# Performance work log

Hardware: AMD Instinct MI355X
Metric: run time of the kernel (lower is better)

Reference implementation:

```python
import math
import jax, jax.numpy as jnp
import numpy as np

B, N, D, H = 2, 2048, 1024, 16
HD = D // H  # 64
TWO_PI = 2.0 * math.pi
ROPE_BASE = 10000.0


def setup_inputs() -> dict:
    key = jax.random.key(0)
    ks = jax.random.split(key, 8)
    s = 0.02
    x = jax.random.normal(ks[0], (B, N, D), dtype=jnp.float32)
    Wq = jax.random.normal(ks[1], (D, D), dtype=jnp.float32) * s
    Wk = jax.random.normal(ks[2], (D, D), dtype=jnp.float32) * s
    Wv = jax.random.normal(ks[3], (D, D), dtype=jnp.float32) * s
    Wo = jax.random.normal(ks[4], (D, D), dtype=jnp.float32) * s
    cw = jax.random.normal(ks[5], (D,), dtype=jnp.float32) * s  # complexity_proj weight
    cb = jnp.zeros((), dtype=jnp.float32)                        # complexity_proj bias
    alpha = jnp.asarray(0.1, dtype=jnp.float32)
    T_base = jnp.asarray(10.0, dtype=jnp.float32)
    root_ids = jax.random.randint(ks[6], (B, N), 0, 1000)
    mask = jnp.tril(jnp.ones((N, N), dtype=jnp.int32))  # causal
    return {"x": x, "Wq": Wq, "Wk": Wk, "Wv": Wv, "Wo": Wo,
            "alpha": alpha, "T_base": T_base, "cw": cw, "cb": cb,
            "root_ids": root_ids, "mask": mask, "t_step": 3}


def _rope_cos_sin(seq_len, head_dim, dtype):
    inv_freq = 1.0 / (ROPE_BASE ** (jnp.arange(0, head_dim, 2, dtype=jnp.float32) / head_dim))
    pos = jnp.arange(seq_len, dtype=jnp.float32)
    freqs = pos[:, None] * inv_freq[None, :]          # (N, HD/2)
    emb = jnp.concatenate([freqs, freqs], axis=-1)    # (N, HD)
    return jnp.cos(emb).astype(dtype), jnp.sin(emb).astype(dtype)


def _rotate_half(t):
    half = t.shape[-1] // 2
    return jnp.concatenate([-t[..., half:], t[..., :half]], axis=-1)


def reference(x, Wq, Wk, Wv, Wo, alpha, T_base, cw, cb, root_ids, mask, t_step):
    b, n, d = x.shape
    # QKV projection -> (B, H, N, HD)
    def proj(W):
        return jnp.einsum('bnd,ed->bne', x, W).reshape(b, n, H, HD).transpose(0, 2, 1, 3)
    q, k, v = proj(Wq), proj(Wk), proj(Wv)
    # RoPE
    cos, sin = _rope_cos_sin(n, HD, x.dtype)          # (N, HD)
    q = q * cos + _rotate_half(q) * sin
    k = k * cos + _rotate_half(k) * sin
    # Per-sample temperature via complexity + cardiac oscillation
    complexity = jax.nn.sigmoid(jnp.einsum('bd,d->b', x.mean(axis=1), cw) + cb)  # (B,)
    T_eff = (jnp.abs(T_base) + 1.0) * (0.5 + complexity)                          # (B,)
    psi = 1.0 + alpha * jnp.sin(TWO_PI * t_step / T_eff)                          # (B,)
    scale = (math.sqrt(HD) * psi)[:, None, None, None]                            # (B,1,1,1)
    # Attention with full NxN scores (eager path, as in source)
    scores = jnp.einsum('bhqd,bhkd->bhqk', q, k) / scale
    scores = jnp.where(mask[None, None, :, :] == 0, -jnp.inf, scores)
    attn = jax.nn.softmax(scores, axis=-1)
    out = jnp.einsum('bhqk,bhkd->bhqd', attn, v)       # (B,H,N,HD)
    out = out.transpose(0, 2, 1, 3).reshape(b, n, d)
    return jnp.einsum('bnd,ed->bne', out, Wo)
```

## Files before the change

### kernel.cpp

```cpp
#include <hip/hip_runtime.h>


typedef short short8 __attribute__((ext_vector_type(8)));
typedef float floatx4 __attribute__((ext_vector_type(4)));
typedef float f32x16 __attribute__((ext_vector_type(16)));
typedef unsigned int uint4v __attribute__((ext_vector_type(4)));
typedef unsigned int u32x4v __attribute__((ext_vector_type(4)));
typedef unsigned short us4 __attribute__((ext_vector_type(4)));
typedef unsigned short u16;

#define DEV __device__ __forceinline__

static const int Bb = 2;

static const size_t OFF_XB = 0;
static const size_t OFF_WQ = 8388608;
static const size_t OFF_WK = OFF_WQ + 2097152;
static const size_t OFF_WV = OFF_WK + 2097152;
static const size_t OFF_WO = OFF_WV + 2097152;
static const size_t OFF_Q  = OFF_WO + 2097152;
static const size_t OFF_K  = OFF_Q + 8388608;
static const size_t OFF_V  = OFF_K + 8388608;
static const size_t OFF_AO = OFF_V + 8388608;
static const size_t OFF_SC = OFF_AO + 8388608;

DEV u16 f2bf(float f) {
  unsigned int u = __builtin_bit_cast(unsigned int, f);
  u += 0x7fffu + ((u >> 16) & 1u);
  return (u16)(u >> 16);
}

DEV unsigned pkbf(float lo, float hi) {
  unsigned r;
  asm("v_cvt_pk_bf16_f32 %0, %1, %2" : "=v"(r) : "v"(lo), "v"(hi));
  return r;
}

__global__ __launch_bounds__(256) void cvt_all_kernel(
    const float* __restrict__ x, const float* __restrict__ wq,
    const float* __restrict__ wk, const float* __restrict__ wv,
    const float* __restrict__ wo, const float* __restrict__ cw,
    u16* __restrict__ xb, u16* __restrict__ wqb, u16* __restrict__ wkb,
    u16* __restrict__ wvb, u16* __restrict__ wob, float* __restrict__ part) {
  const int blk = blockIdx.x;
  if (blk < 4096) {
    int i = blk * 256 + threadIdx.x;
    float4 f = ((const float4*)x)[i];
    us4 o;
    o[0] = f2bf(f.x); o[1] = f2bf(f.y); o[2] = f2bf(f.z); o[3] = f2bf(f.w);
    ((us4*)xb)[i] = o;
    float4 c = ((const float4*)cw)[i & 255];
    float acc = f.x * c.x + f.y * c.y + f.z * c.z + f.w * c.w;
    __shared__ float red[256];
    red[threadIdx.x] = acc;
    __syncthreads();
    for (int s = 128; s > 0; s >>= 1) {
      if (threadIdx.x < s) red[threadIdx.x] += red[threadIdx.x + s];
      __syncthreads();
    }
    if (threadIdx.x == 0) part[blk] = red[0];
  } else {
    int r = blk - 4096;
    int wi = r >> 10;
    int i = (r & 1023) * 256 + threadIdx.x;
    const float* src = (wi == 0) ? wq : (wi == 1) ? wk : (wi == 2) ? wv : wo;
    u16* dst = (wi == 0) ? wqb : (wi == 1) ? wkb : (wi == 2) ? wvb : wob;
    float4 f = ((const float4*)src)[i];
    us4 o;
    o[0] = f2bf(f.x); o[1] = f2bf(f.y); o[2] = f2bf(f.z); o[3] = f2bf(f.w);
    ((us4*)dst)[i] = o;
  }
}

__global__ void scale_finalize_kernel(const float* __restrict__ part,
                                      const float* __restrict__ cb,
                                      const float* __restrict__ alpha,
                                      const float* __restrict__ tb,
                                      const int* __restrict__ tstep,
                                      float* __restrict__ out) {
  const int b = threadIdx.x >> 7, t = threadIdx.x & 127;
  float s = 0.f;
  for (int i = t; i < 2048; i += 128) s += part[b * 2048 + i];
  __shared__ float red[2][128];
  red[b][t] = s;
  __syncthreads();
  for (int st = 64; st > 0; st >>= 1) {
    if (t < st) red[b][t] += red[b][t + st];
    __syncthreads();
  }
  if (t == 0) {
    float sm = red[b][0] * (1.0f / 2048.0f) + cb[0];
    float cx = 1.0f / (1.0f + expf(-sm));
    float Te = (fabsf(tb[0]) + 1.0f) * (0.5f + cx);
    float psi = 1.0f + alpha[0] * sinf(6.283185307179586f * (float)tstep[0] / Te);
    out[b] = 1.0f / (8.0f * psi);
  }
}

__global__ void rope_table_kernel(float2* __restrict__ rt) {
  int i = blockIdx.x * 256 + threadIdx.x;
  int pos = i >> 5, hd2 = i & 31;
  float ang = (float)pos * exp2f(-(float)hd2 * 0.41524101186092030f);
  float sv, cv;
  sincosf(ang, &sv, &cv);
  rt[i] = make_float2(cv, sv);
}

__global__ __launch_bounds__(256) void gemm_qkv_kernel(
    const u16* __restrict__ xb, const u16* __restrict__ wq, const u16* __restrict__ wk,
    const u16* __restrict__ wv, const float2* __restrict__ rt,
    u16* __restrict__ q, u16* __restrict__ k, u16* __restrict__ v) {
  const int tm = blockIdx.x, tn = blockIdx.y, which = blockIdx.z;
  const u16* W = (which == 0) ? wq : (which == 1) ? wk : wv;
  u16* dst = (which == 0) ? q : (which == 1) ? k : v;

  __shared__ __align__(16) u16 As[128 * 32];
  __shared__ __align__(16) u16 Bs[128 * 32];

  const int t = threadIdx.x, lane = t & 63, w = t >> 6;
  const int wm = w >> 1, wn = w & 1, lg = lane >> 4, lr = lane & 15;

  floatx4 acc[4][4];
#pragma unroll
  for (int i = 0; i < 4; i++)
#pragma unroll
    for (int j = 0; j < 4; j++) acc[i][j] = (floatx4){0.f, 0.f, 0.f, 0.f};

  const int rowA = tm * 128, rowB = tn * 128;
  for (int kt = 0; kt < 32; ++kt) {
#pragma unroll
    for (int s = 0; s < 2; s++) {
      int c = t + s * 256;
      int r = c >> 2, kc = c & 3;
      *(uint4v*)(As + r * 32 + kc * 8) =
          *(const uint4v*)(xb + (size_t)(rowA + r) * 1024 + kt * 32 + kc * 8);
      *(uint4v*)(Bs + r * 32 + kc * 8) =
          *(const uint4v*)(W + (size_t)(rowB + r) * 1024 + kt * 32 + kc * 8);
    }
    __syncthreads();
    short8 af[4], bw[4];
#pragma unroll
    for (int i = 0; i < 4; i++)
      af[i] = *(const short8*)(As + (wm * 64 + i * 16 + lr) * 32 + lg * 8);
#pragma unroll
    for (int j = 0; j < 4; j++)
      bw[j] = *(const short8*)(Bs + (wn * 64 + j * 16 + lr) * 32 + lg * 8);
#pragma unroll
    for (int i = 0; i < 4; i++)
#pragma unroll
      for (int j = 0; j < 4; j++)
        acc[i][j] = __builtin_amdgcn_mfma_f32_16x16x32_bf16(af[i], bw[j], acc[i][j], 0, 0, 0);
    __syncthreads();
  }

  const int rowbase = tm * 128 + wm * 64, colbase = tn * 128 + wn * 64;
  if (which <= 1) {
#pragma unroll
    for (int i = 0; i < 4; i++)
#pragma unroll
      for (int ii = 0; ii < 4; ii++) {
        int gm = rowbase + i * 16 + lg * 4 + ii;
        int pos = gm & 2047, bb = gm >> 11;
#pragma unroll
        for (int jp = 0; jp < 2; jp++) {
          int hd2 = jp * 16 + lr;
          float2 cs = rt[pos * 32 + hd2];
          float a0 = acc[i][jp][ii], a1 = acc[i][jp + 2][ii];
          int e0 = colbase + jp * 16 + lr;
          int hh = e0 >> 6;
          size_t base = (((size_t)bb * 16 + hh) * 2048 + pos) * 64;
          dst[base + hd2]      = f2bf(a0 * cs.x - a1 * cs.y);
          dst[base + hd2 + 32] = f2bf(a1 * cs.x + a0 * cs.y);
        }
      }
  } else {
#pragma unroll
    for (int i = 0; i < 4; i++)
#pragma unroll
      for (int ii = 0; ii < 4; ii++) {
        int gm = rowbase + i * 16 + lg * 4 + ii;
        int pos = gm & 2047, bb = gm >> 11;
#pragma unroll
        for (int j = 0; j < 4; j++) {
          int ge = colbase + j * 16 + lr;
          int hh = ge >> 6, hd = ge & 63;
          dst[(((size_t)bb * 16 + hh) * 2048 + pos) * 64 + hd] = f2bf(acc[i][j][ii]);
        }
      }
  }
}

__global__ __launch_bounds__(256) void vtrans_kernel(const u16* __restrict__ v,
                                                     u16* __restrict__ vt) {
  const int bh = blockIdx.x, nt = blockIdx.y;
  __shared__ __align__(16) u16 T[64 * 64];
  const int t = threadIdx.x;
  const size_t vi = (size_t)bh * 131072 + (size_t)nt * 4096;
#pragma unroll
  for (int s = 0; s < 2; s++) {
    int g = s * 256 + t, n = g >> 3, dc = g & 7;
    *(uint4v*)(T + n * 64 + ((dc ^ (n & 7)) * 8)) =
        *(const uint4v*)(v + vi + (size_t)n * 64 + dc * 8);
  }
  __syncthreads();
  const size_t vo = (size_t)bh * 131072 + (size_t)nt * 64;
#pragma unroll
  for (int s = 0; s < 2; s++) {
    int g = s * 256 + t, nc = g & 7, d = g >> 3;
    short8 o;
#pragma unroll
    for (int jj = 0; jj < 8; jj++) {
      int n = nc * 8 + jj;
      o[jj] = (short)T[n * 64 + (((d >> 3) ^ (n & 7)) * 8) + (d & 7)];
    }
    *(short8*)(vt + vo + (size_t)d * 2048 + nc * 8) = o;
  }
}

__global__ __launch_bounds__(512, 2) void attn_kernel(
    const u16* __restrict__ q, const u16* __restrict__ k, const u16* __restrict__ vt,
    u16* __restrict__ ao, const float* __restrict__ scale_ws) {
  const int bid = blockIdx.x;
  const int swz = (bid & 7) * 64 + (bid >> 3);
  const int bh = swz >> 4, p = swz & 15;
  const int b = bh >> 4, h = bh & 15;
  const int w = threadIdx.x >> 6, lane = threadIdx.x & 63;
  const int l31 = lane & 31, hi = lane >> 5;
  const int w4 = w & 3, sp = w >> 2;
  const int tsel = (w4 == 0) ? p : (w4 == 1) ? 31 - p : (w4 == 2) ? 32 + p : 63 - p;
  const int q0 = tsel * 32;
  const int KT = tsel >> 1;
  const float isc2 = scale_ws[b] * 1.4426950408889634f;
  const size_t koff = (size_t)bh * 131072;
  const float NINF = -__builtin_inff();

  __shared__ float Olds[4][64][33];
  __shared__ float Mlds[4][2][32];

  short8 bq[4];
#pragma unroll
  for (int k4 = 0; k4 < 4; k4++)
    bq[k4] = *(const short8*)(q + koff + (size_t)(q0 + l31) * 64 + k4 * 16 + hi * 8);

  f32x16 o0, o1;
#pragma unroll
  for (int r = 0; r < 16; r++) { o0[r] = 0.f; o1[r] = 0.f; }
  float m2 = NINF, ell = 0.f;

  for (int kt = sp; kt <= KT; kt += 2) {
    const int cbase = kt << 6;
    const bool haveMt1 = (cbase + 32 <= q0 + 31);

    short8 ka0[4], ka1[4];
#pragma unroll
    for (int k4 = 0; k4 < 4; k4++)
      ka0[k4] = *(const short8*)(k + koff + (size_t)(cbase + l31) * 64 + k4 * 16 + hi * 8);
    if (haveMt1) {
#pragma unroll
      for (int k4 = 0; k4 < 4; k4++)
        ka1[k4] = *(const short8*)(k + koff + (size_t)(cbase + 32 + l31) * 64 + k4 * 16 + hi * 8);
    }
    const int nct = haveMt1 ? 4 : 2;
    short8 va0[4], va1[4];
#pragma unroll
    for (int ct = 0; ct < 4; ct++) {
      if (ct < nct) {
        va0[ct] = *(const short8*)(vt + koff + (size_t)l31 * 2048 + cbase + ct * 16 + hi * 8);
        va1[ct] = *(const short8*)(vt + koff + (size_t)(32 + l31) * 2048 + cbase + ct * 16 + hi * 8);
      }
    }

    f32x16 s0, s1;
#pragma unroll
    for (int r = 0; r < 16; r++) { s0[r] = 0.f; s1[r] = 0.f; }
#pragma unroll
    for (int k4 = 0; k4 < 4; k4++)
      s0 = __builtin_amdgcn_mfma_f32_32x32x16_bf16(ka0[k4], bq[k4], s0, 0, 0, 0);
    if (haveMt1) {
#pragma unroll
      for (int k4 = 0; k4 < 4; k4++)
        s1 = __builtin_amdgcn_mfma_f32_32x32x16_bf16(ka1[k4], bq[k4], s1, 0, 0, 0);
    }

#pragma unroll
    for (int r = 0; r < 16; r++) { s0[r] *= isc2; s1[r] *= isc2; }
    if (kt == KT) {
      const int thr = q0 + l31 - cbase;
#pragma unroll
      for (int r = 0; r < 16; r++) {
        const int crow = (r & 3) + 8 * (r >> 2) + 4 * hi;
        if (crow > thr) s0[r] = NINF;
        if (crow + 32 > thr) s1[r] = NINF;
      }
    }

    float mx = s0[0];
#pragma unroll
    for (int r = 1; r < 16; r++) mx = fmaxf(mx, s0[r]);
#pragma unroll
    for (int r = 0; r < 16; r++) mx = fmaxf(mx, s1[r]);
    mx = fmaxf(mx, __shfl_xor(mx, 32, 64));
    const float mn = fmaxf(m2, mx);
    const float rsc = exp2f(m2 - mn);
    m2 = mn;
    f32x16 p0, p1;
    float ps = 0.f;
#pragma unroll
    for (int r = 0; r < 16; r++) { p0[r] = exp2f(s0[r] - mn); ps += p0[r]; }
#pragma unroll
    for (int r = 0; r < 16; r++) { p1[r] = exp2f(s1[r] - mn); ps += p1[r]; }
    ps += __shfl_xor(ps, 32, 64);
    ell = ell * rsc + ps;
#pragma unroll
    for (int r = 0; r < 16; r++) { o0[r] *= rsc; o1[r] *= rsc; }

#pragma unroll
    for (int ct = 0; ct < 4; ct++) {
      if (ct < nct) {
        const f32x16& pp = (ct < 2) ? p0 : p1;
        const int rA = (ct & 1) * 8;
        unsigned pkA0 = pkbf(pp[rA + 0], pp[rA + 1]);
        unsigned pkA1 = pkbf(pp[rA + 2], pp[rA + 3]);
        unsigned pkB0 = pkbf(pp[rA + 4], pp[rA + 5]);
        unsigned pkB1 = pkbf(pp[rA + 6], pp[rA + 7]);
        unsigned u0 = (unsigned)__shfl_xor((int)(hi ? pkA0 : pkB0), 32, 64);
        unsigned u1 = (unsigned)__shfl_xor((int)(hi ? pkA1 : pkB1), 32, 64);
        u32x4v pu;
        pu[0] = hi ? u0 : pkA0;
        pu[1] = hi ? u1 : pkA1;
        pu[2] = hi ? pkB0 : u0;
        pu[3] = hi ? pkB1 : u1;
        short8 pf = __builtin_bit_cast(short8, pu);
        o0 = __builtin_amdgcn_mfma_f32_32x32x16_bf16(va0[ct], pf, o0, 0, 0, 0);
        o1 = __builtin_amdgcn_mfma_f32_32x32x16_bf16(va1[ct], pf, o1, 0, 0, 0);
      }
    }
  }

  if (w >= 4) {
#pragma unroll
    for (int r = 0; r < 16; r++) {
      Olds[w4][2 * r + hi][l31]      = o0[r];
      Olds[w4][32 + 2 * r + hi][l31] = o1[r];
    }
    if (hi == 0) { Mlds[w4][0][l31] = m2; Mlds[w4][1][l31] = ell; }
  }
  __syncthreads();
  if (w < 4) {
    const float m_hi = Mlds[w4][0][l31], l_hi = Mlds[w4][1][l31];
    const float mN = fmaxf(m2, m_hi);
    const float w0 = exp2f(m2 - mN), w1 = exp2f(m_hi - mN);
    const float invl = 1.0f / (w0 * ell + w1 * l_hi);
    u16* orow = ao + ((size_t)(b * 2048 + q0 + l31)) * 1024 + h * 64;
#pragma unroll
    for (int qd = 0; qd < 4; qd++) {
      us4 st0, st1;
#pragma unroll
      for (int j = 0; j < 4; j++) {
        int r = qd * 4 + j;
        st0[j] = f2bf((w0 * o0[r] + w1 * Olds[w4][2 * r + hi][l31]) * invl);
        st1[j] = f2bf((w0 * o1[r] + w1 * Olds[w4][32 + 2 * r + hi][l31]) * invl);
      }
      *(us4*)(orow + qd * 8 + hi * 4) = st0;
      *(us4*)(orow + 32 + qd * 8 + hi * 4) = st1;
    }
  }
}

__global__ __launch_bounds__(256) void gemm_out_kernel(const u16* __restrict__ ab,
                                                       const u16* __restrict__ wo,
                                                       float* __restrict__ out) {
  const int tm = blockIdx.x, tn = blockIdx.y;
  __shared__ __align__(16) u16 As[128 * 32];
  __shared__ __align__(16) u16 Bs[128 * 32];

  const int t = threadIdx.x, lane = t & 63, w = t >> 6;
  const int wm = w >> 1, wn = w & 1, lg = lane >> 4, lr = lane & 15;

  floatx4 acc[4][4];
#pragma unroll
  for (int i = 0; i < 4; i++)
#pragma unroll
    for (int j = 0; j < 4; j++) acc[i][j] = (floatx4){0.f, 0.f, 0.f, 0.f};

  const int rowA = tm * 128, rowB = tn * 128;
  for (int kt = 0; kt < 32; ++kt) {
#pragma unroll
    for (int s = 0; s < 2; s++) {
      int c = t + s * 256;
      int r = c >> 2, kc = c & 3;
      *(uint4v*)(As + r * 32 + kc * 8) =
          *(const uint4v*)(ab + (size_t)(rowA + r) * 1024 + kt * 32 + kc * 8);
      *(uint4v*)(Bs + r * 32 + kc * 8) =
          *(const uint4v*)(wo + (size_t)(rowB + r) * 1024 + kt * 32 + kc * 8);
    }
    __syncthreads();
    short8 af[4], bw[4];
#pragma unroll
    for (int i = 0; i < 4; i++)
      af[i] = *(const short8*)(As + (wm * 64 + i * 16 + lr) * 32 + lg * 8);
#pragma unroll
    for (int j = 0; j < 4; j++)
      bw[j] = *(const short8*)(Bs + (wn * 64 + j * 16 + lr) * 32 + lg * 8);
#pragma unroll
    for (int i = 0; i < 4; i++)
#pragma unroll
      for (int j = 0; j < 4; j++)
        acc[i][j] = __builtin_amdgcn_mfma_f32_16x16x32_bf16(af[i], bw[j], acc[i][j], 0, 0, 0);
    __syncthreads();
  }

  const int rowbase = tm * 128 + wm * 64, colbase = tn * 128 + wn * 64;
#pragma unroll
  for (int i = 0; i < 4; i++)
#pragma unroll
    for (int ii = 0; ii < 4; ii++) {
      int gm = rowbase + i * 16 + lg * 4 + ii;
#pragma unroll
      for (int j = 0; j < 4; j++) {
        int ge = colbase + j * 16 + lr;
        out[(size_t)gm * 1024 + ge] = acc[i][j][ii];
      }
    }
}

extern "C" void kernel_launch(void* const* d_in, const int* in_sizes, int n_in,
                              void* d_out, int out_size, void* d_ws, size_t ws_size,
                              hipStream_t stream) {
  const float* x     = (const float*)d_in[0];
  const float* Wq    = (const float*)d_in[1];
  const float* Wk    = (const float*)d_in[2];
  const float* Wv    = (const float*)d_in[3];
  const float* Wo    = (const float*)d_in[4];
  const float* alpha = (const float*)d_in[5];
  const float* Tb    = (const float*)d_in[6];
  const float* cw    = (const float*)d_in[7];
  const float* cb    = (const float*)d_in[8];
  const int*   tstep = (const int*)d_in[11];

  char* ws = (char*)d_ws;
  u16* xb  = (u16*)(ws + OFF_XB);
  u16* wqb = (u16*)(ws + OFF_WQ);
  u16* wkb = (u16*)(ws + OFF_WK);
  u16* wvb = (u16*)(ws + OFF_WV);
  u16* wob = (u16*)(ws + OFF_WO);
  u16* qb  = (u16*)(ws + OFF_Q);
  u16* kb  = (u16*)(ws + OFF_K);
  u16* vb  = (u16*)(ws + OFF_V);
  u16* aob = (u16*)(ws + OFF_AO);
  u16* vtb = (u16*)(ws + OFF_XB);
  float2* rt = (float2*)(ws + OFF_AO);
  float* sc = (float*)(ws + OFF_SC);
  float* part = sc + 4;

  cvt_all_kernel<<<8192, 256, 0, stream>>>(x, Wq, Wk, Wv, Wo, cw,
                                           xb, wqb, wkb, wvb, wob, part);
  scale_finalize_kernel<<<1, 256, 0, stream>>>(part, cb, alpha, Tb, tstep, sc);
  rope_table_kernel<<<256, 256, 0, stream>>>(rt);

  gemm_qkv_kernel<<<dim3(32, 8, 3), 256, 0, stream>>>(xb, wqb, wkb, wvb, rt, qb, kb, vb);

  vtrans_kernel<<<dim3(32, 32), 256, 0, stream>>>(vb, vtb);

  attn_kernel<<<dim3(512), 512, 0, stream>>>(qb, kb, vtb, aob, sc);

  gemm_out_kernel<<<dim3(32, 8), 256, 0, stream>>>(aob, wob, (float*)d_out);
}
```

Measured before the change: 271.9 us.

## Drop split-K in attention, add lazy rescale and MFMA priority, merge prep kernels

The attention kernel no longer splits each query tile's key range across two wave groups. Blocks shrink to 256 threads with one wave per query tile, which removes the LDS merge and block-wide barrier. The online-softmax rescale is now skipped unless some lane's max grows by more than 8 (log2 units), and s_setprio is raised around the MFMA sections. The scale-finalize and RoPE-table kernels are merged into one launch. In exchange each wave walks twice as many key tiles serially, so the kernel has less parallelism and a longer critical path, and the lazy rescale leaves exponent values up to 2^8 before normalisation.

```diff
diff --git a/kernel.cpp b/kernel.cpp
--- a/kernel.cpp
+++ b/kernel.cpp
@@ -72,38 +72,38 @@
   }
 }
 
-__global__ void scale_finalize_kernel(const float* __restrict__ part,
-                                      const float* __restrict__ cb,
-                                      const float* __restrict__ alpha,
-                                      const float* __restrict__ tb,
-                                      const int* __restrict__ tstep,
-                                      float* __restrict__ out) {
-  const int b = threadIdx.x >> 7, t = threadIdx.x & 127;
-  float s = 0.f;
-  for (int i = t; i < 2048; i += 128) s += part[b * 2048 + i];
-  __shared__ float red[2][128];
-  red[b][t] = s;
-  __syncthreads();
-  for (int st = 64; st > 0; st >>= 1) {
-    if (t < st) red[b][t] += red[b][t + st];
-    __syncthreads();
-  }
-  if (t == 0) {
-    float sm = red[b][0] * (1.0f / 2048.0f) + cb[0];
-    float cx = 1.0f / (1.0f + expf(-sm));
-    float Te = (fabsf(tb[0]) + 1.0f) * (0.5f + cx);
-    float psi = 1.0f + alpha[0] * sinf(6.283185307179586f * (float)tstep[0] / Te);
-    out[b] = 1.0f / (8.0f * psi);
-  }
-}
-
-__global__ void rope_table_kernel(float2* __restrict__ rt) {
-  int i = blockIdx.x * 256 + threadIdx.x;
-  int pos = i >> 5, hd2 = i & 31;
-  float ang = (float)pos * exp2f(-(float)hd2 * 0.41524101186092030f);
-  float sv, cv;
-  sincosf(ang, &sv, &cv);
-  rt[i] = make_float2(cv, sv);
+__global__ void prep_kernel(const float* __restrict__ part,
+                            const float* __restrict__ cb,
+                            const float* __restrict__ alpha,
+                            const float* __restrict__ tb,
+                            const int* __restrict__ tstep,
+                            float* __restrict__ out, float2* __restrict__ rt) {
+  if (blockIdx.x == 256) {
+    const int b = threadIdx.x >> 7, t = threadIdx.x & 127;
+    float s = 0.f;
+    for (int i = t; i < 2048; i += 128) s += part[b * 2048 + i];
+    __shared__ float red[2][128];
+    red[b][t] = s;
+    __syncthreads();
+    for (int st = 64; st > 0; st >>= 1) {
+      if (t < st) red[b][t] += red[b][t + st];
+      __syncthreads();
+    }
+    if (t == 0) {
+      float sm = red[b][0] * (1.0f / 2048.0f) + cb[0];
+      float cx = 1.0f / (1.0f + expf(-sm));
+      float Te = (fabsf(tb[0]) + 1.0f) * (0.5f + cx);
+      float psi = 1.0f + alpha[0] * sinf(6.283185307179586f * (float)tstep[0] / Te);
+      out[b] = 1.0f / (8.0f * psi);
+    }
+  } else {
+    int i = blockIdx.x * 256 + threadIdx.x;
+    int pos = i >> 5, hd2 = i & 31;
+    float ang = (float)pos * exp2f(-(float)hd2 * 0.41524101186092030f);
+    float sv, cv;
+    sincosf(ang, &sv, &cv);
+    rt[i] = make_float2(cv, sv);
+  }
 }
 
 __global__ __launch_bounds__(256) void gemm_qkv_kernel(
@@ -217,7 +217,7 @@
   }
 }
 
-__global__ __launch_bounds__(512, 2) void attn_kernel(
+__global__ __launch_bounds__(256) void attn_kernel(
     const u16* __restrict__ q, const u16* __restrict__ k, const u16* __restrict__ vt,
     u16* __restrict__ ao, const float* __restrict__ scale_ws) {
   const int bid = blockIdx.x;
@@ -226,17 +226,13 @@
   const int b = bh >> 4, h = bh & 15;
   const int w = threadIdx.x >> 6, lane = threadIdx.x & 63;
   const int l31 = lane & 31, hi = lane >> 5;
-  const int w4 = w & 3, sp = w >> 2;
-  const int tsel = (w4 == 0) ? p : (w4 == 1) ? 31 - p : (w4 == 2) ? 32 + p : 63 - p;
+  const int tsel = (w == 0) ? p : (w == 1) ? 31 - p : (w == 2) ? 32 + p : 63 - p;
   const int q0 = tsel * 32;
   const int KT = tsel >> 1;
   const float isc2 = scale_ws[b] * 1.4426950408889634f;
   const size_t koff = (size_t)bh * 131072;
   const float NINF = -__builtin_inff();
 
-  __shared__ float Olds[4][64][33];
-  __shared__ float Mlds[4][2][32];
-
   short8 bq[4];
 #pragma unroll
   for (int k4 = 0; k4 < 4; k4++)
@@ -247,7 +243,7 @@
   for (int r = 0; r < 16; r++) { o0[r] = 0.f; o1[r] = 0.f; }
   float m2 = NINF, ell = 0.f;
 
-  for (int kt = sp; kt <= KT; kt += 2) {
+  for (int kt = 0; kt <= KT; ++kt) {
     const int cbase = kt << 6;
     const bool haveMt1 = (cbase + 32 <= q0 + 31);
 
@@ -273,6 +269,7 @@
     f32x16 s0, s1;
 #pragma unroll
     for (int r = 0; r < 16; r++) { s0[r] = 0.f; s1[r] = 0.f; }
+    __builtin_amdgcn_s_setprio(1);
 #pragma unroll
     for (int k4 = 0; k4 < 4; k4++)
       s0 = __builtin_amdgcn_mfma_f32_32x32x16_bf16(ka0[k4], bq[k4], s0, 0, 0, 0);
@@ -281,6 +278,7 @@
       for (int k4 = 0; k4 < 4; k4++)
         s1 = __builtin_amdgcn_mfma_f32_32x32x16_bf16(ka1[k4], bq[k4], s1, 0, 0, 0);
     }
+    __builtin_amdgcn_s_setprio(0);
 
 #pragma unroll
     for (int r = 0; r < 16; r++) { s0[r] *= isc2; s1[r] *= isc2; }
@@ -300,20 +298,24 @@
 #pragma unroll
     for (int r = 0; r < 16; r++) mx = fmaxf(mx, s1[r]);
     mx = fmaxf(mx, __shfl_xor(mx, 32, 64));
-    const float mn = fmaxf(m2, mx);
-    const float rsc = exp2f(m2 - mn);
-    m2 = mn;
+    if (!__all(mx <= m2 + 8.0f)) {
+      const float mn = fmaxf(m2, mx);
+      const float rsc = exp2f(m2 - mn);
+      m2 = mn;
+      ell *= rsc;
+#pragma unroll
+      for (int r = 0; r < 16; r++) { o0[r] *= rsc; o1[r] *= rsc; }
+    }
     f32x16 p0, p1;
     float ps = 0.f;
 #pragma unroll
-    for (int r = 0; r < 16; r++) { p0[r] = exp2f(s0[r] - mn); ps += p0[r]; }
-#pragma unroll
-    for (int r = 0; r < 16; r++) { p1[r] = exp2f(s1[r] - mn); ps += p1[r]; }
+    for (int r = 0; r < 16; r++) { p0[r] = exp2f(s0[r] - m2); ps += p0[r]; }
+#pragma unroll
+    for (int r = 0; r < 16; r++) { p1[r] = exp2f(s1[r] - m2); ps += p1[r]; }
     ps += __shfl_xor(ps, 32, 64);
-    ell = ell * rsc + ps;
-#pragma unroll
-    for (int r = 0; r < 16; r++) { o0[r] *= rsc; o1[r] *= rsc; }
-
+    ell += ps;
+
+    __builtin_amdgcn_s_setprio(1);
 #pragma unroll
     for (int ct = 0; ct < 4; ct++) {
       if (ct < nct) {
@@ -335,35 +337,21 @@
         o1 = __builtin_amdgcn_mfma_f32_32x32x16_bf16(va1[ct], pf, o1, 0, 0, 0);
       }
     }
-  }
-
-  if (w >= 4) {
-#pragma unroll
-    for (int r = 0; r < 16; r++) {
-      Olds[w4][2 * r + hi][l31]      = o0[r];
-      Olds[w4][32 + 2 * r + hi][l31] = o1[r];
-    }
-    if (hi == 0) { Mlds[w4][0][l31] = m2; Mlds[w4][1][l31] = ell; }
-  }
-  __syncthreads();
-  if (w < 4) {
-    const float m_hi = Mlds[w4][0][l31], l_hi = Mlds[w4][1][l31];
-    const float mN = fmaxf(m2, m_hi);
-    const float w0 = exp2f(m2 - mN), w1 = exp2f(m_hi - mN);
-    const float invl = 1.0f / (w0 * ell + w1 * l_hi);
-    u16* orow = ao + ((size_t)(b * 2048 + q0 + l31)) * 1024 + h * 64;
-#pragma unroll
-    for (int qd = 0; qd < 4; qd++) {
-      us4 st0, st1;
-#pragma unroll
-      for (int j = 0; j < 4; j++) {
-        int r = qd * 4 + j;
-        st0[j] = f2bf((w0 * o0[r] + w1 * Olds[w4][2 * r + hi][l31]) * invl);
-        st1[j] = f2bf((w0 * o1[r] + w1 * Olds[w4][32 + 2 * r + hi][l31]) * invl);
-      }
-      *(us4*)(orow + qd * 8 + hi * 4) = st0;
-      *(us4*)(orow + 32 + qd * 8 + hi * 4) = st1;
-    }
+    __builtin_amdgcn_s_setprio(0);
+  }
+
+  const float invl = 1.0f / ell;
+  u16* orow = ao + ((size_t)(b * 2048 + q0 + l31)) * 1024 + h * 64;
+#pragma unroll
+  for (int qd = 0; qd < 4; qd++) {
+    us4 st0, st1;
+#pragma unroll
+    for (int j = 0; j < 4; j++) {
+      st0[j] = f2bf(o0[qd * 4 + j] * invl);
+      st1[j] = f2bf(o1[qd * 4 + j] * invl);
+    }
+    *(us4*)(orow + qd * 8 + hi * 4) = st0;
+    *(us4*)(orow + 32 + qd * 8 + hi * 4) = st1;
   }
 }
 
@@ -455,14 +443,13 @@
 
   cvt_all_kernel<<<8192, 256, 0, stream>>>(x, Wq, Wk, Wv, Wo, cw,
                                            xb, wqb, wkb, wvb, wob, part);
-  scale_finalize_kernel<<<1, 256, 0, stream>>>(part, cb, alpha, Tb, tstep, sc);
-  rope_table_kernel<<<256, 256, 0, stream>>>(rt);
+  prep_kernel<<<257, 256, 0, stream>>>(part, cb, alpha, Tb, tstep, sc, rt);
 
   gemm_qkv_kernel<<<dim3(32, 8, 3), 256, 0, stream>>>(xb, wqb, wkb, wvb, rt, qb, kb, vb);
 
   vtrans_kernel<<<dim3(32, 32), 256, 0, stream>>>(vb, vtb);
 
-  attn_kernel<<<dim3(512), 512, 0, stream>>>(qb, kb, vtb, aob, sc);
+  attn_kernel<<<dim3(512), 256, 0, stream>>>(qb, kb, vtb, aob, sc);
 
   gemm_out_kernel<<<dim3(32, 8), 256, 0, stream>>>(aob, wob, (float*)d_out);
 }
```

Result: slower. 299.2 us (+10.0%).
